# Performance work log

Hardware: AMD Instinct MI355X
Metric: run time of the kernel (lower is better)

Reference implementation:

```python
import jax, jax.numpy as jnp
import numpy as np

N_HEAD = 16

def setup_inputs() -> dict:
    key = jax.random.key(0)
    ks = jax.random.split(key, 5)
    C = 1024
    x = jax.random.normal(ks[0], (2, 2048, C), dtype=jnp.float32)
    W_qkv = jax.random.normal(ks[1], (C, 3 * C), dtype=jnp.float32) * (C ** -0.5)
    b_qkv = jnp.zeros((3 * C,), dtype=jnp.float32)
    W_proj = jax.random.normal(ks[2], (C, C), dtype=jnp.float32) * (C ** -0.5)
    b_proj = jnp.zeros((C,), dtype=jnp.float32)
    return {"x": x, "W_qkv": W_qkv, "b_qkv": b_qkv, "W_proj": W_proj, "b_proj": b_proj}

def reference(x, W_qkv, b_qkv, W_proj, b_proj):
    B, T, C = x.shape
    H = N_HEAD
    D = C // H
    scale = D ** -0.5
    qkv = x @ W_qkv + b_qkv                      # [B,T,3C]
    q, k, v = jnp.split(qkv, 3, axis=-1)
    # [B,T,C] -> [B,H,T,D]
    q = q.reshape(B, T, H, D).transpose(0, 2, 1, 3)
    k = k.reshape(B, T, H, D).transpose(0, 2, 1, 3)
    v = v.reshape(B, T, H, D).transpose(0, 2, 1, 3)
    attn = jnp.einsum('bhqd,bhkd->bhqk', q, k) * scale   # [B,H,T,T]
    causal = jnp.tril(jnp.ones((T, T), dtype=bool))
    attn = jnp.where(causal, attn, -jnp.inf)
    attn = jax.nn.softmax(attn, axis=-1)
    y = jnp.einsum('bhqk,bhkd->bhqd', attn, v)           # [B,H,T,D]
    y = y.transpose(0, 2, 1, 3).reshape(B, T, C)
    return y @ W_proj + b_proj
```

## Files before the change

kernel.cpp:

```cpp
#include <hip/hip_runtime.h>

typedef __attribute__((ext_vector_type(8))) _Float16 h8;
typedef __attribute__((ext_vector_type(4))) float f4;

#define QKSCALE 0.18033688011112042f

__global__ __launch_bounds__(256) void cast_f16_kernel(const float* __restrict__ in,
                                                       _Float16* __restrict__ out, int n) {
  int i = (blockIdx.x * 256 + threadIdx.x) * 8;
  if (i >= n) return;
  const float4* p = (const float4*)(in + i);
  float4 a = p[0], b = p[1];
  h8 v;
  v[0] = (_Float16)a.x; v[1] = (_Float16)a.y; v[2] = (_Float16)a.z; v[3] = (_Float16)a.w;
  v[4] = (_Float16)b.x; v[5] = (_Float16)b.y; v[6] = (_Float16)b.z; v[7] = (_Float16)b.w;
  *(h8*)(out + i) = v;
}

__global__ __launch_bounds__(256) void transp_cast_kernel(const float* __restrict__ W,
                                                          _Float16* __restrict__ Wt, int K, int N) {
  __shared__ _Float16 tile[64][72];
  int k0 = blockIdx.y * 64, n0 = blockIdx.x * 64;
  int t = threadIdx.x;
#pragma unroll
  for (int i = 0; i < 16; ++i) {
    int idx = i * 256 + t;
    int kr = idx >> 6, nc = idx & 63;
    tile[kr][nc] = (_Float16)W[(size_t)(k0 + kr) * N + n0 + nc];
  }
  __syncthreads();
#pragma unroll
  for (int i = 0; i < 2; ++i) {
    int idx = i * 256 + t;
    int nr = idx >> 3, kc = (idx & 7) * 8;
    h8 v;
#pragma unroll
    for (int j = 0; j < 8; ++j) v[j] = tile[kc + j][nr];
    *(h8*)&Wt[(size_t)(n0 + nr) * K + k0 + kc] = v;
  }
}

template <int MODE>
__global__ __launch_bounds__(256) void gemm_f16(const _Float16* __restrict__ A,
                                                const _Float16* __restrict__ Bt,
                                                const float* __restrict__ bias,
                                                float* __restrict__ outF,
                                                _Float16* __restrict__ oQ,
                                                _Float16* __restrict__ oK,
                                                _Float16* __restrict__ oV,
                                                int M, int N, int K) {
  __shared__ _Float16 As[128 * 64];
  __shared__ _Float16 Bs[128 * 64];
  const int m0 = blockIdx.y * 128, n0 = blockIdx.x * 128;
  const int tid = threadIdx.x;
  const int wave = tid >> 6, lane = tid & 63;
  const int wr = (wave >> 1) * 64, wc = (wave & 1) * 64;
  const int lrow = lane & 15, g = lane >> 4;
  f4 acc[4][4];
  const f4 z4 = {0.f, 0.f, 0.f, 0.f};
#pragma unroll
  for (int m = 0; m < 4; ++m)
#pragma unroll
    for (int n = 0; n < 4; ++n) acc[m][n] = z4;

  for (int k0 = 0; k0 < K; k0 += 64) {
#pragma unroll
    for (int i = 0; i < 4; ++i) {
      int L = i * 256 + tid;
      int row = L >> 3, c = L & 7;
      int cs = (c ^ (row & 7)) * 8;
      *(h8*)&As[row * 64 + c * 8] = *(const h8*)&A[(size_t)(m0 + row) * K + k0 + cs];
      *(h8*)&Bs[row * 64 + c * 8] = *(const h8*)&Bt[(size_t)(n0 + row) * K + k0 + cs];
    }
    __syncthreads();
#pragma unroll
    for (int ss = 0; ss < 2; ++ss) {
      h8 af[4], bf[4];
#pragma unroll
      for (int m = 0; m < 4; ++m) {
        int row = wr + m * 16 + lrow;
        af[m] = *(const h8*)&As[row * 64 + (((ss * 4 + g) ^ (row & 7)) * 8)];
      }
#pragma unroll
      for (int n = 0; n < 4; ++n) {
        int row = wc + n * 16 + lrow;
        bf[n] = *(const h8*)&Bs[row * 64 + (((ss * 4 + g) ^ (row & 7)) * 8)];
      }
#pragma unroll
      for (int m = 0; m < 4; ++m)
#pragma unroll
        for (int n = 0; n < 4; ++n)
          acc[m][n] = __builtin_amdgcn_mfma_f32_16x16x32_f16(af[m], bf[n], acc[m][n], 0, 0, 0);
    }
    __syncthreads();
  }

#pragma unroll
  for (int n = 0; n < 4; ++n) {
    const int gcol = n0 + wc + n * 16 + lrow;
    const float bv = bias ? bias[gcol] : 0.f;
#pragma unroll
    for (int m = 0; m < 4; ++m) {
#pragma unroll
      for (int r = 0; r < 4; ++r) {
        const int grow = m0 + wr + m * 16 + g * 4 + r;
        float v = acc[m][n][r] + bv;
        if (MODE == 0) {
          outF[(size_t)grow * N + gcol] = v;
        } else {
          int part = gcol >> 10;
          int c1 = gcol & 1023;
          int hh = c1 >> 6, d = c1 & 63;
          int b = grow >> 11, t = grow & 2047;
          int bh = b * 16 + hh;
          if (part == 0)
            oQ[((size_t)bh * 2048 + t) * 64 + d] = (_Float16)(v * QKSCALE);
          else if (part == 1)
            oK[((size_t)bh * 2048 + t) * 64 + d] = (_Float16)v;
          else
            oV[((size_t)bh * 64 + d) * 2048 + t] = (_Float16)v;
        }
      }
    }
  }
}

__global__ __launch_bounds__(256) void attn_kernel(const _Float16* __restrict__ Qg,
                                                   const _Float16* __restrict__ Kg,
                                                   const _Float16* __restrict__ Vtg,
                                                   _Float16* __restrict__ Og) {
  __shared__ _Float16 plds[4][32][72];
  __shared__ float obuf[4][32][65];
  __shared__ float mlds[2][4][32];

  const int idx = blockIdx.x;
  const int bh = (idx & 7) | (((idx >> 3) & 3) << 3);
  const int qt2 = 63 - (idx >> 5);
  const int q0 = qt2 * 32;

  const int wave = threadIdx.x >> 6, lane = threadIdx.x & 63;
  const int lrow = lane & 15, g = lane >> 4;
  const int b = bh >> 4, h = bh & 15;
  const _Float16* Q = Qg + (size_t)bh * 2048 * 64;
  const _Float16* K = Kg + (size_t)bh * 2048 * 64;
  const _Float16* Vt = Vtg + (size_t)bh * 64 * 2048;

  h8 aq[2][2];
#pragma unroll
  for (int mt = 0; mt < 2; ++mt)
#pragma unroll
    for (int ss = 0; ss < 2; ++ss)
      aq[mt][ss] = *(const h8*)&Q[(q0 + mt * 16 + lrow) * 64 + ss * 32 + g * 8];

  const f4 z4 = {0.f, 0.f, 0.f, 0.f};
  f4 o[2][4];
#pragma unroll
  for (int mt = 0; mt < 2; ++mt)
#pragma unroll
    for (int dt = 0; dt < 4; ++dt) o[mt][dt] = z4;
  float mrow[2][4], lsum[2][4];
#pragma unroll
  for (int mt = 0; mt < 2; ++mt)
#pragma unroll
    for (int r = 0; r < 4; ++r) { mrow[mt][r] = -1e30f; lsum[mt][r] = 0.f; }

  _Float16(*pw)[72] = plds[wave];
  const int NT = (qt2 >> 1) + 1;

  for (int it = wave; it < NT; it += 4) {
    const int kv0 = it * 64;
    h8 kf[4][2], vf[4][2];
#pragma unroll
    for (int ct = 0; ct < 4; ++ct)
#pragma unroll
      for (int ss = 0; ss < 2; ++ss)
        kf[ct][ss] = *(const h8*)&K[(kv0 + ct * 16 + lrow) * 64 + ss * 32 + g * 8];
#pragma unroll
    for (int dt = 0; dt < 4; ++dt)
#pragma unroll
      for (int ss = 0; ss < 2; ++ss)
        vf[dt][ss] = *(const h8*)&Vt[(size_t)(dt * 16 + lrow) * 2048 + kv0 + ss * 32 + g * 8];

    f4 s[2][4];
#pragma unroll
    for (int mt = 0; mt < 2; ++mt)
#pragma unroll
      for (int ct = 0; ct < 4; ++ct) s[mt][ct] = z4;
#pragma unroll
    for (int ss = 0; ss < 2; ++ss)
#pragma unroll
      for (int mt = 0; mt < 2; ++mt)
#pragma unroll
        for (int ct = 0; ct < 4; ++ct)
          s[mt][ct] = __builtin_amdgcn_mfma_f32_16x16x32_f16(aq[mt][ss], kf[ct][ss], s[mt][ct], 0, 0, 0);

    if (it == NT - 1) {
#pragma unroll
      for (int mt = 0; mt < 2; ++mt)
#pragma unroll
        for (int ct = 0; ct < 4; ++ct)
#pragma unroll
          for (int r = 0; r < 4; ++r)
            if (kv0 + ct * 16 + lrow > q0 + mt * 16 + g * 4 + r) s[mt][ct][r] = -1e30f;
    }

#pragma unroll
    for (int mt = 0; mt < 2; ++mt)
#pragma unroll
      for (int r = 0; r < 4; ++r) {
        float pm = fmaxf(fmaxf(s[mt][0][r], s[mt][1][r]), fmaxf(s[mt][2][r], s[mt][3][r]));
        pm = fmaxf(pm, __shfl_xor(pm, 1));
        pm = fmaxf(pm, __shfl_xor(pm, 2));
        pm = fmaxf(pm, __shfl_xor(pm, 4));
        pm = fmaxf(pm, __shfl_xor(pm, 8));
        float mn = fmaxf(mrow[mt][r], pm);
        float fr = __builtin_amdgcn_exp2f(mrow[mt][r] - mn);
        mrow[mt][r] = mn;
        float ps = 0.f;
#pragma unroll
        for (int ct = 0; ct < 4; ++ct) {
          float p = __builtin_amdgcn_exp2f(s[mt][ct][r] - mn);
          s[mt][ct][r] = p;
          ps += p;
        }
        ps += __shfl_xor(ps, 1);
        ps += __shfl_xor(ps, 2);
        ps += __shfl_xor(ps, 4);
        ps += __shfl_xor(ps, 8);
        lsum[mt][r] = lsum[mt][r] * fr + ps;
#pragma unroll
        for (int dt = 0; dt < 4; ++dt) o[mt][dt][r] *= fr;
      }

#pragma unroll
    for (int mt = 0; mt < 2; ++mt)
#pragma unroll
      for (int ct = 0; ct < 4; ++ct)
#pragma unroll
        for (int r = 0; r < 4; ++r)
          pw[mt * 16 + g * 4 + r][ct * 16 + lrow] = (_Float16)s[mt][ct][r];

    h8 ap[2][2];
#pragma unroll
    for (int mt = 0; mt < 2; ++mt)
#pragma unroll
      for (int ss = 0; ss < 2; ++ss)
        ap[mt][ss] = *(const h8*)&pw[mt * 16 + lrow][ss * 32 + g * 8];

#pragma unroll
    for (int ss = 0; ss < 2; ++ss)
#pragma unroll
      for (int mt = 0; mt < 2; ++mt)
#pragma unroll
        for (int dt = 0; dt < 4; ++dt)
          o[mt][dt] = __builtin_amdgcn_mfma_f32_16x16x32_f16(ap[mt][ss], vf[dt][ss], o[mt][dt], 0, 0, 0);
  }

  if (lrow == 0) {
#pragma unroll
    for (int mt = 0; mt < 2; ++mt)
#pragma unroll
      for (int r = 0; r < 4; ++r) {
        mlds[0][wave][mt * 16 + g * 4 + r] = mrow[mt][r];
        mlds[1][wave][mt * 16 + g * 4 + r] = lsum[mt][r];
      }
  }
#pragma unroll
  for (int mt = 0; mt < 2; ++mt)
#pragma unroll
    for (int dt = 0; dt < 4; ++dt)
#pragma unroll
      for (int r = 0; r < 4; ++r)
        obuf[wave][mt * 16 + g * 4 + r][dt * 16 + lrow] = o[mt][dt][r];
  __syncthreads();

  {
    const int ql = threadIdx.x >> 3;
    const int d0 = (threadIdx.x & 7) * 8;
    float m0 = mlds[0][0][ql], m1 = mlds[0][1][ql], m2 = mlds[0][2][ql], m3 = mlds[0][3][ql];
    float M = fmaxf(fmaxf(m0, m1), fmaxf(m2, m3));
    float f0 = __builtin_amdgcn_exp2f(m0 - M);
    float f1 = __builtin_amdgcn_exp2f(m1 - M);
    float f2 = __builtin_amdgcn_exp2f(m2 - M);
    float f3 = __builtin_amdgcn_exp2f(m3 - M);
    float l = f0 * mlds[1][0][ql] + f1 * mlds[1][1][ql] + f2 * mlds[1][2][ql] + f3 * mlds[1][3][ql];
    float inv = 1.f / l;
    h8 outv;
#pragma unroll
    for (int j = 0; j < 8; ++j) {
      float v = f0 * obuf[0][ql][d0 + j] + f1 * obuf[1][ql][d0 + j] +
                f2 * obuf[2][ql][d0 + j] + f3 * obuf[3][ql][d0 + j];
      outv[j] = (_Float16)(v * inv);
    }
    *(h8*)&Og[((size_t)b * 2048 + q0 + ql) * 1024 + h * 64 + d0] = outv;
  }
}

extern "C" void kernel_launch(void* const* d_in, const int* in_sizes, int n_in,
                              void* d_out, int out_size, void* d_ws, size_t ws_size,
                              hipStream_t stream) {
  const float* x = (const float*)d_in[0];
  const float* Wqkv = (const float*)d_in[1];
  const float* bqkv = (const float*)d_in[2];
  const float* Wproj = (const float*)d_in[3];
  const float* bproj = (const float*)d_in[4];
  float* out = (float*)d_out;

  char* ws = (char*)d_ws;
  const size_t MB = 1u << 20;
  _Float16* xh     = (_Float16*)(ws + 0 * MB);
  _Float16* wqkvt  = (_Float16*)(ws + 8 * MB);
  _Float16* wprojt = (_Float16*)(ws + 14 * MB);
  _Float16* qh     = (_Float16*)(ws + 16 * MB);
  _Float16* kh     = (_Float16*)(ws + 24 * MB);
  _Float16* vth    = (_Float16*)(ws + 32 * MB);
  _Float16* oh     = (_Float16*)(ws + 40 * MB);

  cast_f16_kernel<<<2048, 256, 0, stream>>>(x, xh, 4194304);
  transp_cast_kernel<<<dim3(48, 16), 256, 0, stream>>>(Wqkv, wqkvt, 1024, 3072);
  transp_cast_kernel<<<dim3(16, 16), 256, 0, stream>>>(Wproj, wprojt, 1024, 1024);

  gemm_f16<1><<<dim3(24, 32), 256, 0, stream>>>(xh, wqkvt, bqkv, nullptr, qh, kh, vth,
                                                4096, 3072, 1024);
  attn_kernel<<<dim3(2048), 256, 0, stream>>>(qh, kh, vth, oh);
  gemm_f16<0><<<dim3(8, 32), 256, 0, stream>>>(oh, wprojt, bproj, out, nullptr, nullptr, nullptr,
                                               4096, 1024, 1024);
}
```

Measured before the change: 162.7 us.

## Add lazy softmax rescale, defer row-sum reduction, shrink LDS via fp16 merge slab

The per-tile max shuffle-reduction and the rescale of O and l now run only when some row's max grows by more than a threshold (wave-wide __any vote), so most tiles skip the cross-lane reductions and the exp for the rescale factor. Row sums are kept as lane partials and reduced once after the loop. Each wave's normalized O is written in fp16 into the reused P slab instead of a separate fp32 obuf, which cuts LDS use and lets launch_bounds request 4 blocks per CU. The costs are a stale running max (bounded by the threshold, so p values can reach 2^8 before rescaling) and some extra precision loss in the fp16 cross-wave merge.

```diff
diff --git a/kernel.cpp b/kernel.cpp
--- a/kernel.cpp
+++ b/kernel.cpp
@@ -125,12 +125,11 @@
   }
 }
 
-__global__ __launch_bounds__(256) void attn_kernel(const _Float16* __restrict__ Qg,
-                                                   const _Float16* __restrict__ Kg,
-                                                   const _Float16* __restrict__ Vtg,
-                                                   _Float16* __restrict__ Og) {
-  __shared__ _Float16 plds[4][32][72];
-  __shared__ float obuf[4][32][65];
+__global__ __launch_bounds__(256, 4) void attn_kernel(const _Float16* __restrict__ Qg,
+                                                      const _Float16* __restrict__ Kg,
+                                                      const _Float16* __restrict__ Vtg,
+                                                      _Float16* __restrict__ Og) {
+  __shared__ _Float16 slab[4][32][72];
   __shared__ float mlds[2][4][32];
 
   const int idx = blockIdx.x;
@@ -158,13 +157,13 @@
   for (int mt = 0; mt < 2; ++mt)
 #pragma unroll
     for (int dt = 0; dt < 4; ++dt) o[mt][dt] = z4;
-  float mrow[2][4], lsum[2][4];
-#pragma unroll
-  for (int mt = 0; mt < 2; ++mt)
-#pragma unroll
-    for (int r = 0; r < 4; ++r) { mrow[mt][r] = -1e30f; lsum[mt][r] = 0.f; }
-
-  _Float16(*pw)[72] = plds[wave];
+  float mrow[2][4], lpart[2][4];
+#pragma unroll
+  for (int mt = 0; mt < 2; ++mt)
+#pragma unroll
+    for (int r = 0; r < 4; ++r) { mrow[mt][r] = -1e30f; lpart[mt][r] = 0.f; }
+
+  _Float16(*pw)[72] = slab[wave];
   const int NT = (qt2 >> 1) + 1;
 
   for (int it = wave; it < NT; it += 4) {
@@ -204,41 +203,46 @@
             if (kv0 + ct * 16 + lrow > q0 + mt * 16 + g * 4 + r) s[mt][ct][r] = -1e30f;
     }
 
+    float pm[2][4];
+    bool need = false;
 #pragma unroll
     for (int mt = 0; mt < 2; ++mt)
 #pragma unroll
       for (int r = 0; r < 4; ++r) {
-        float pm = fmaxf(fmaxf(s[mt][0][r], s[mt][1][r]), fmaxf(s[mt][2][r], s[mt][3][r]));
-        pm = fmaxf(pm, __shfl_xor(pm, 1));
-        pm = fmaxf(pm, __shfl_xor(pm, 2));
-        pm = fmaxf(pm, __shfl_xor(pm, 4));
-        pm = fmaxf(pm, __shfl_xor(pm, 8));
-        float mn = fmaxf(mrow[mt][r], pm);
-        float fr = __builtin_amdgcn_exp2f(mrow[mt][r] - mn);
-        mrow[mt][r] = mn;
+        pm[mt][r] = fmaxf(fmaxf(s[mt][0][r], s[mt][1][r]), fmaxf(s[mt][2][r], s[mt][3][r]));
+        need = need || (pm[mt][r] > mrow[mt][r] + 8.f);
+      }
+    if (__any(need)) {
+#pragma unroll
+      for (int mt = 0; mt < 2; ++mt)
+#pragma unroll
+        for (int r = 0; r < 4; ++r) {
+          float m = pm[mt][r];
+          m = fmaxf(m, __shfl_xor(m, 1));
+          m = fmaxf(m, __shfl_xor(m, 2));
+          m = fmaxf(m, __shfl_xor(m, 4));
+          m = fmaxf(m, __shfl_xor(m, 8));
+          float mn = fmaxf(mrow[mt][r], m);
+          float fr = __builtin_amdgcn_exp2f(mrow[mt][r] - mn);
+          mrow[mt][r] = mn;
+          lpart[mt][r] *= fr;
+#pragma unroll
+          for (int dt = 0; dt < 4; ++dt) o[mt][dt][r] *= fr;
+        }
+    }
+#pragma unroll
+    for (int mt = 0; mt < 2; ++mt)
+#pragma unroll
+      for (int r = 0; r < 4; ++r) {
         float ps = 0.f;
 #pragma unroll
         for (int ct = 0; ct < 4; ++ct) {
-          float p = __builtin_amdgcn_exp2f(s[mt][ct][r] - mn);
-          s[mt][ct][r] = p;
+          float p = __builtin_amdgcn_exp2f(s[mt][ct][r] - mrow[mt][r]);
           ps += p;
+          pw[mt * 16 + g * 4 + r][ct * 16 + lrow] = (_Float16)p;
         }
-        ps += __shfl_xor(ps, 1);
-        ps += __shfl_xor(ps, 2);
-        ps += __shfl_xor(ps, 4);
-        ps += __shfl_xor(ps, 8);
-        lsum[mt][r] = lsum[mt][r] * fr + ps;
-#pragma unroll
-        for (int dt = 0; dt < 4; ++dt) o[mt][dt][r] *= fr;
-      }
-
-#pragma unroll
-    for (int mt = 0; mt < 2; ++mt)
-#pragma unroll
-      for (int ct = 0; ct < 4; ++ct)
-#pragma unroll
-        for (int r = 0; r < 4; ++r)
-          pw[mt * 16 + g * 4 + r][ct * 16 + lrow] = (_Float16)s[mt][ct][r];
+        lpart[mt][r] += ps;
+      }
 
     h8 ap[2][2];
 #pragma unroll
@@ -256,22 +260,36 @@
           o[mt][dt] = __builtin_amdgcn_mfma_f32_16x16x32_f16(ap[mt][ss], vf[dt][ss], o[mt][dt], 0, 0, 0);
   }
 
+#pragma unroll
+  for (int mt = 0; mt < 2; ++mt)
+#pragma unroll
+    for (int r = 0; r < 4; ++r) {
+      float l = lpart[mt][r];
+      l += __shfl_xor(l, 1);
+      l += __shfl_xor(l, 2);
+      l += __shfl_xor(l, 4);
+      l += __shfl_xor(l, 8);
+      lpart[mt][r] = l;
+    }
+
   if (lrow == 0) {
 #pragma unroll
     for (int mt = 0; mt < 2; ++mt)
 #pragma unroll
       for (int r = 0; r < 4; ++r) {
         mlds[0][wave][mt * 16 + g * 4 + r] = mrow[mt][r];
-        mlds[1][wave][mt * 16 + g * 4 + r] = lsum[mt][r];
-      }
-  }
-#pragma unroll
-  for (int mt = 0; mt < 2; ++mt)
-#pragma unroll
-    for (int dt = 0; dt < 4; ++dt)
-#pragma unroll
-      for (int r = 0; r < 4; ++r)
-        obuf[wave][mt * 16 + g * 4 + r][dt * 16 + lrow] = o[mt][dt][r];
+        mlds[1][wave][mt * 16 + g * 4 + r] = lpart[mt][r];
+      }
+  }
+#pragma unroll
+  for (int mt = 0; mt < 2; ++mt)
+#pragma unroll
+    for (int r = 0; r < 4; ++r) {
+      float inv = lpart[mt][r] > 0.f ? 1.f / lpart[mt][r] : 0.f;
+#pragma unroll
+      for (int dt = 0; dt < 4; ++dt)
+        pw[mt * 16 + g * 4 + r][dt * 16 + lrow] = (_Float16)(o[mt][dt][r] * inv);
+    }
   __syncthreads();
 
   {
@@ -279,17 +297,19 @@
     const int d0 = (threadIdx.x & 7) * 8;
     float m0 = mlds[0][0][ql], m1 = mlds[0][1][ql], m2 = mlds[0][2][ql], m3 = mlds[0][3][ql];
     float M = fmaxf(fmaxf(m0, m1), fmaxf(m2, m3));
-    float f0 = __builtin_amdgcn_exp2f(m0 - M);
-    float f1 = __builtin_amdgcn_exp2f(m1 - M);
-    float f2 = __builtin_amdgcn_exp2f(m2 - M);
-    float f3 = __builtin_amdgcn_exp2f(m3 - M);
-    float l = f0 * mlds[1][0][ql] + f1 * mlds[1][1][ql] + f2 * mlds[1][2][ql] + f3 * mlds[1][3][ql];
-    float inv = 1.f / l;
+    float f0 = __builtin_amdgcn_exp2f(m0 - M) * mlds[1][0][ql];
+    float f1 = __builtin_amdgcn_exp2f(m1 - M) * mlds[1][1][ql];
+    float f2 = __builtin_amdgcn_exp2f(m2 - M) * mlds[1][2][ql];
+    float f3 = __builtin_amdgcn_exp2f(m3 - M) * mlds[1][3][ql];
+    float inv = 1.f / (f0 + f1 + f2 + f3);
+    h8 o0 = *(const h8*)&slab[0][ql][d0];
+    h8 o1 = *(const h8*)&slab[1][ql][d0];
+    h8 o2 = *(const h8*)&slab[2][ql][d0];
+    h8 o3 = *(const h8*)&slab[3][ql][d0];
     h8 outv;
 #pragma unroll
     for (int j = 0; j < 8; ++j) {
-      float v = f0 * obuf[0][ql][d0 + j] + f1 * obuf[1][ql][d0 + j] +
-                f2 * obuf[2][ql][d0 + j] + f3 * obuf[3][ql][d0 + j];
+      float v = f0 * (float)o0[j] + f1 * (float)o1[j] + f2 * (float)o2[j] + f3 * (float)o3[j];
       outv[j] = (_Float16)(v * inv);
     }
     *(h8*)&Og[((size_t)b * 2048 + q0 + ql) * 1024 + h * 64 + d0] = outv;
```

Measured after the change: 224.6 us. 1.38x slower.
